# Optimization experiments

Hardware: AMD Instinct MI355X
Metric: run time of the kernel (lower is better)

## Reference

```python
import jax, jax.numpy as jnp
import numpy as np

N_NODES = 100000
N_EDGES = 1600000
IN_DIM, HID_DIM, OUT_DIM = 128, 256, 128


def setup_inputs() -> dict:
    key = jax.random.key(0)
    ks = jax.random.split(key, 5)
    x = jax.random.normal(ks[0], (N_NODES, IN_DIM), dtype=jnp.float32)
    src = jax.random.randint(ks[1], (N_EDGES,), 0, N_NODES, dtype=jnp.int64)
    dst = jax.random.randint(ks[2], (N_EDGES,), 0, N_NODES, dtype=jnp.int64)
    # Glorot-ish init for linear weights (DGL GraphConv default), zero bias
    W1 = jax.random.normal(ks[3], (IN_DIM, HID_DIM), dtype=jnp.float32) * (1.0 / np.sqrt(IN_DIM))
    W2 = jax.random.normal(ks[4], (HID_DIM, OUT_DIM), dtype=jnp.float32) * (1.0 / np.sqrt(HID_DIM))
    b1 = jnp.zeros((HID_DIM,), dtype=jnp.float32)
    b2 = jnp.zeros((OUT_DIM,), dtype=jnp.float32)
    return {"x": x, "src": src, "dst": dst, "W1": W1, "b1": b1, "W2": W2, "b2": b2}


def _degree_norms(src, dst, n_nodes):
    # norm='both': D_out(src)^{-1/2} on messages, D_in(dst)^{-1/2} on aggregate;
    # degrees clamped to min 1 as in DGL.
    ones = jnp.ones(src.shape[0], dtype=jnp.float32)
    deg_out = jax.ops.segment_sum(ones, src, num_segments=n_nodes)
    deg_in = jax.ops.segment_sum(ones, dst, num_segments=n_nodes)
    norm_src = jax.lax.rsqrt(jnp.maximum(deg_out, 1.0))
    norm_dst = jax.lax.rsqrt(jnp.maximum(deg_in, 1.0))
    return norm_src, norm_dst


def _graph_conv(x, src, dst, W, b, norm_src, norm_dst):
    h = x * norm_src[:, None]                                  # [N, d]
    agg = jax.ops.segment_sum(h[src], dst, num_segments=x.shape[0])  # [N, d]
    agg = agg * norm_dst[:, None]
    return agg @ W + b


def reference(x, src, dst, W1, b1, W2, b2):
    norm_src, norm_dst = _degree_norms(src, dst, x.shape[0])
    h = jax.nn.relu(_graph_conv(x, src, dst, W1, b1, norm_src, norm_dst))
    out = _graph_conv(h, src, dst, W2, b2, norm_src, norm_dst)
    return out
```

## Files before the change

kernel.cpp:

```cpp
#include <hip/hip_runtime.h>

constexpr int N_NODES = 100000;
constexpr int N_EDGES = 1600000;
constexpr int DIN = 128, DHID = 256, DOUT = 128;

constexpr int NB = 256;
constexpr int BR = 391;
constexpr int CAP = 8192;
constexpr int NBLK1 = 256;
constexpr int CHUNK = (N_EDGES + NBLK1 - 1) / NBLK1;

typedef __bf16 bf16x8 __attribute__((ext_vector_type(8)));
typedef float f32x4 __attribute__((ext_vector_type(4)));

static __device__ __forceinline__ ushort f2bf(float f) {
    uint u = __float_as_uint(f);
    uint r = (u + 0x7FFFu + ((u >> 16) & 1u)) >> 16;
    return (ushort)r;
}
static __device__ __forceinline__ float bf2f(ushort h) {
    return __uint_as_float(((uint)h) << 16);
}
static __device__ __forceinline__ float bflo(uint w) { return __uint_as_float(w << 16); }
static __device__ __forceinline__ float bfhi(uint w) { return __uint_as_float(w & 0xFFFF0000u); }

__global__ __launch_bounds__(512) void part_kernel(const int* __restrict__ src,
                                                   const int* __restrict__ dst,
                                                   int* __restrict__ curA, int* __restrict__ curB,
                                                   uint* __restrict__ ppair,
                                                   ushort* __restrict__ psv, int e,
                                                   const float* __restrict__ W1,
                                                   ushort* __restrict__ Wf1,
                                                   const float* __restrict__ W2,
                                                   ushort* __restrict__ Wf2) {
    const int t = threadIdx.x;
    if (blockIdx.x >= NBLK1) {
        int i = (blockIdx.x - NBLK1) * 512 + t;
        if (i < DIN * DHID) {
            int frag = i >> 9, r = i & 511;
            int lane = r >> 3, ee = r & 7;
            int kb = frag & 3, ii = (frag >> 2) & 1, w = (frag >> 3) & 3, kh = frag >> 5;
            int c = w * 32 + ii * 16 + (lane & 15);
            int k = kb * 32 + (lane >> 4) * 8 + ee;
            Wf1[i] = f2bf(W1[k * DHID + kh * 128 + c]);
        } else {
            int i2 = i - DIN * DHID;
            int frag = i2 >> 9, r = i2 & 511;
            int lane = r >> 3, ee = r & 7;
            int kb2 = frag & 3, j2 = (frag >> 2) & 1, w = (frag >> 3) & 3, kh = frag >> 5;
            int c2 = w * 32 + j2 * 16 + (lane & 15);
            int k2 = kh * 128 + kb2 * 32 + (lane >> 4) * 8 + ee;
            Wf2[i2] = f2bf(W2[k2 * DOUT + c2]);
        }
        return;
    }
    __shared__ int hA[NB], hB[NB], rA[NB], rB[NB], cA[NB], cB[NB];
    const int b0 = blockIdx.x * CHUNK;
    const int cnt = min(e - b0, CHUNK);
    if (t < NB) { hA[t] = 0; hB[t] = 0; cA[t] = 0; cB[t] = 0; }
    __syncthreads();
    for (int i = t; i < cnt; i += 512) {
        int s = src[b0 + i], d = dst[b0 + i];
        atomicAdd(&hA[d / BR], 1);
        atomicAdd(&hB[s / BR], 1);
    }
    __syncthreads();
    if (t < NB) {
        rA[t] = atomicAdd(&curA[t], hA[t]);
        rB[t] = atomicAdd(&curB[t], hB[t]);
    }
    __syncthreads();
    for (int i = t; i < cnt; i += 512) {
        int s = src[b0 + i], d = dst[b0 + i];
        int bd = d / BR;
        int bs = s / BR;
        int p = rA[bd] + atomicAdd(&cA[bd], 1);
        if (p < CAP) ppair[(size_t)bd * CAP + p] = ((uint)(d - bd * BR) << 17) | (uint)s;
        int q = rB[bs] + atomicAdd(&cB[bs], 1);
        if (q < CAP) psv[(size_t)bs * CAP + q] = (ushort)(s - bs * BR);
    }
}

__global__ __launch_bounds__(512) void csrn_kernel(const int* __restrict__ curA,
                                                   const int* __restrict__ curB,
                                                   const uint* __restrict__ ppair,
                                                   const ushort* __restrict__ psv,
                                                   int* __restrict__ csr,
                                                   int* __restrict__ rowstart,
                                                   float* __restrict__ ndst,
                                                   float* __restrict__ nsrc,
                                                   const float* __restrict__ x,
                                                   ushort* __restrict__ xb, int n, int e) {
    __shared__ uint ploc[CAP];
    __shared__ int hist[512], sc[512], exc[512], cur[512];
    __shared__ int sbst;
    const int t = threadIdx.x;
    const int b = blockIdx.x & 255;
    const int side = blockIdx.x >> 8;
    const int first = b * BR;
    const int nr = min(BR, n - first);
    const size_t base = (size_t)b * CAP;

    if (side == 0) {
        const int cntA = min(curA[b], CAP);
        if (t < 256) sc[t] = curA[t];
        __syncthreads();
        for (int off = 1; off < 256; off <<= 1) {
            int add = 0;
            if (t < 256 && t >= off) add = sc[t - off];
            __syncthreads();
            if (t < 256) sc[t] += add;
            __syncthreads();
        }
        if (t == 0) {
            sbst = (b == 0) ? 0 : sc[b - 1];
            if (b == 0) rowstart[n] = e;
        }
        hist[t] = 0;
        cur[t] = 0;
        __syncthreads();
        const int bst = sbst;

        for (int i = t; i < cntA; i += 512) {
            uint p = ppair[base + i];
            ploc[i] = p;
            atomicAdd(&hist[p >> 17], 1);
        }
        __syncthreads();
        int h = hist[t];
        sc[t] = h;
        __syncthreads();
        for (int off = 1; off < 512; off <<= 1) {
            int add = (t >= off) ? sc[t - off] : 0;
            __syncthreads();
            sc[t] += add;
            __syncthreads();
        }
        exc[t] = sc[t] - h;
        if (t < nr) {
            rowstart[first + t] = bst + exc[t];
            ndst[first + t] = rsqrtf(fmaxf((float)h, 1.0f));
        }
        __syncthreads();
        for (int i = t; i < cntA; i += 512) {
            uint p = ploc[i];
            int dl = p >> 17;
            int pos = exc[dl] + atomicAdd(&cur[dl], 1);
            csr[bst + pos] = (int)(p & 0x1FFFFu);
        }
    } else {
        if (nr <= 0) return;
        hist[t] = 0;
        __syncthreads();
        const int cntB = min(curB[b], CAP);
        for (int i = t; i < cntB; i += 512) atomicAdd(&hist[psv[base + i]], 1);
        __syncthreads();
        float* nsv = (float*)exc;
        if (t < nr) {
            float v = rsqrtf(fmaxf((float)hist[t], 1.0f));
            nsrc[first + t] = v;
            nsv[t] = v;
        }
        __syncthreads();
        const int rl = t >> 5, q = t & 31;
        for (int i = rl; i < nr; i += 16) {
            float s = nsv[i];
            const size_t ro = (size_t)(first + i) * 128;
            float4 v = *(const float4*)&x[ro + q * 4];
            ushort4 o = {f2bf(v.x * s), f2bf(v.y * s), f2bf(v.z * s), f2bf(v.w * s)};
            *(ushort4*)&xb[ro + q * 4] = o;
        }
    }
}

template <bool OUTBF16, bool ADDBIAS>
__global__ __launch_bounds__(256) void aggh_kernel(const ushort* __restrict__ Xb,
                                                   const int* __restrict__ csr,
                                                   const int* __restrict__ rowstart,
                                                   const float* __restrict__ ndst,
                                                   const float* __restrict__ bias,
                                                   float* __restrict__ outf,
                                                   ushort* __restrict__ outb, int n, int half) {
    int g = threadIdx.x >> 3;
    int lane = threadIdx.x & 7;
    int d = blockIdx.x * 32 + g;
    if (d >= n) return;
    int beg = rowstart[d], end = rowstart[d + 1];
    const int fo = half * 64 + lane * 8;
    const ushort* Xp = Xb + fo;
    float acc[8];
#pragma unroll
    for (int j = 0; j < 8; j++) acc[j] = 0.f;

#define ACC8(v)                                   \
    do {                                          \
        acc[0] += bflo(v.x); acc[1] += bfhi(v.x); \
        acc[2] += bflo(v.y); acc[3] += bfhi(v.y); \
        acc[4] += bflo(v.z); acc[5] += bfhi(v.z); \
        acc[6] += bflo(v.w); acc[7] += bfhi(v.w); \
    } while (0)

    int k = beg;
    for (; k + 4 <= end; k += 4) {
        int s0 = csr[k], s1 = csr[k + 1], s2 = csr[k + 2], s3 = csr[k + 3];
        uint4 v0 = *(const uint4*)(Xp + (size_t)s0 * 128);
        uint4 v1 = *(const uint4*)(Xp + (size_t)s1 * 128);
        uint4 v2 = *(const uint4*)(Xp + (size_t)s2 * 128);
        uint4 v3 = *(const uint4*)(Xp + (size_t)s3 * 128);
        ACC8(v0);
        ACC8(v1);
        ACC8(v2);
        ACC8(v3);
    }
    for (; k < end; ++k) {
        uint4 v = *(const uint4*)(Xp + (size_t)csr[k] * 128);
        ACC8(v);
    }
#undef ACC8

    float nd = ndst[d];
#pragma unroll
    for (int j = 0; j < 8; j++) acc[j] *= nd;
    if constexpr (ADDBIAS) {
        float4 b0 = *(const float4*)&bias[fo];
        float4 b1 = *(const float4*)&bias[fo + 4];
        acc[0] += b0.x; acc[1] += b0.y; acc[2] += b0.z; acc[3] += b0.w;
        acc[4] += b1.x; acc[5] += b1.y; acc[6] += b1.z; acc[7] += b1.w;
    }
    if constexpr (OUTBF16) {
        uint4 o;
        o.x = (uint)f2bf(acc[0]) | ((uint)f2bf(acc[1]) << 16);
        o.y = (uint)f2bf(acc[2]) | ((uint)f2bf(acc[3]) << 16);
        o.z = (uint)f2bf(acc[4]) | ((uint)f2bf(acc[5]) << 16);
        o.w = (uint)f2bf(acc[6]) | ((uint)f2bf(acc[7]) << 16);
        *(uint4*)(outb + (size_t)d * 128 + fo) = o;
    } else {
        float4 o0 = {acc[0], acc[1], acc[2], acc[3]};
        float4 o1 = {acc[4], acc[5], acc[6], acc[7]};
        *(float4*)(outf + (size_t)d * 128 + fo) = o0;
        *(float4*)(outf + (size_t)d * 128 + fo + 4) = o1;
    }
}

__global__ __launch_bounds__(256) void fused64_kernel(const ushort* __restrict__ A,
                                                      const ushort* __restrict__ Wf1,
                                                      const float* __restrict__ b1,
                                                      const float* __restrict__ nsrc,
                                                      const ushort* __restrict__ Wf2,
                                                      ushort* __restrict__ T, int M) {
    __shared__ ushort Sa[64][128];
    __shared__ ushort H1[64][128];
    const int row0 = blockIdx.x * 64;
    const int t = threadIdx.x;
    const int w = t >> 6, lane = t & 63;
    const int l16 = lane & 15, lk = lane >> 4;

    float nsv[4];
#pragma unroll
    for (int j = 0; j < 4; j++) {
        int gm = row0 + j * 16 + l16;
        nsv[j] = nsrc[gm < M ? gm : (M - 1)];
    }
    float4 bvv[2][2];
#pragma unroll
    for (int kh = 0; kh < 2; kh++)
#pragma unroll
        for (int i = 0; i < 2; i++)
            bvv[kh][i] = *(const float4*)&b1[kh * 128 + w * 32 + i * 16 + lk * 4];

#pragma unroll
    for (int i = 0; i < 4; i++) {
        int idx = i * 256 + t;
        int r = idx >> 4, oct = idx & 15;
        int gr = row0 + r;
        uint4 v = make_uint4(0u, 0u, 0u, 0u);
        if (gr < M) v = *(const uint4*)&A[(size_t)gr * 128 + oct * 8];
        *(uint4*)((char*)&Sa[0][0] + r * 256 + (oct ^ (r & 15)) * 16) = v;
    }
    __syncthreads();

    f32x4 acc2[4][2];
#pragma unroll
    for (int i = 0; i < 4; i++)
#pragma unroll
        for (int j = 0; j < 2; j++) acc2[i][j] = (f32x4){0.f, 0.f, 0.f, 0.f};

    for (int kh = 0; kh < 2; kh++) {
        const ushort* w1p = Wf1 + ((size_t)(kh * 4 + w) * 8) * 512 + lane * 8;
        const ushort* w2p = Wf2 + ((size_t)(kh * 4 + w) * 8) * 512 + lane * 8;
        bf16x8 af[2][4], wb[2][4];
#pragma unroll
        for (int i = 0; i < 2; i++)
#pragma unroll
            for (int kb = 0; kb < 4; kb++) af[i][kb] = *(const bf16x8*)(w1p + (i * 4 + kb) * 512);
#pragma unroll
        for (int j2 = 0; j2 < 2; j2++)
#pragma unroll
            for (int kb2 = 0; kb2 < 4; kb2++)
                wb[j2][kb2] = *(const bf16x8*)(w2p + (j2 * 4 + kb2) * 512);

        f32x4 acc1[2][4];
#pragma unroll
        for (int i = 0; i < 2; i++)
#pragma unroll
            for (int j = 0; j < 4; j++) acc1[i][j] = (f32x4){0.f, 0.f, 0.f, 0.f};

#pragma unroll
        for (int kb = 0; kb < 4; kb++) {
            bf16x8 bf_[4];
#pragma unroll
            for (int j = 0; j < 4; j++) {
                int m = j * 16 + l16;
                bf_[j] = *(const bf16x8*)((const char*)&Sa[0][0] + m * 256 +
                                          ((kb * 4 + lk) ^ l16) * 16);
            }
#pragma unroll
            for (int i = 0; i < 2; i++)
#pragma unroll
                for (int j = 0; j < 4; j++)
                    acc1[i][j] =
                        __builtin_amdgcn_mfma_f32_16x16x32_bf16(af[i][kb], bf_[j], acc1[i][j], 0, 0, 0);
        }
        __syncthreads();

#pragma unroll
        for (int i = 0; i < 2; i++) {
            int cb = w * 32 + i * 16 + lk * 4;
            float4 bv = bvv[kh][i];
#pragma unroll
            for (int j = 0; j < 4; j++) {
                int m = j * 16 + l16;
                float ns = nsv[j];
                ushort4 pk;
                pk.x = f2bf(fmaxf(acc1[i][j][0] + bv.x, 0.f) * ns);
                pk.y = f2bf(fmaxf(acc1[i][j][1] + bv.y, 0.f) * ns);
                pk.z = f2bf(fmaxf(acc1[i][j][2] + bv.z, 0.f) * ns);
                pk.w = f2bf(fmaxf(acc1[i][j][3] + bv.w, 0.f) * ns);
                int oct = cb >> 3;
                *(ushort4*)((char*)&H1[0][0] + m * 256 + ((oct ^ l16) & 15) * 16 +
                            (cb & 7) * 2) = pk;
            }
        }
        __syncthreads();

#pragma unroll
        for (int kb2 = 0; kb2 < 4; kb2++) {
            bf16x8 ha[4];
#pragma unroll
            for (int i2 = 0; i2 < 4; i2++) {
                int m = i2 * 16 + l16;
                ha[i2] = *(const bf16x8*)((const char*)&H1[0][0] + m * 256 +
                                          ((kb2 * 4 + lk) ^ l16) * 16);
            }
#pragma unroll
            for (int i2 = 0; i2 < 4; i2++)
#pragma unroll
                for (int j2 = 0; j2 < 2; j2++)
                    acc2[i2][j2] = __builtin_amdgcn_mfma_f32_16x16x32_bf16(ha[i2], wb[j2][kb2],
                                                                           acc2[i2][j2], 0, 0, 0);
        }
    }

#pragma unroll
    for (int i2 = 0; i2 < 4; i2++) {
#pragma unroll
        for (int j2 = 0; j2 < 2; j2++) {
#pragma unroll
            for (int q = 0; q < 4; q++) {
                int r = row0 + i2 * 16 + lk * 4 + q;
                int c = w * 32 + j2 * 16 + l16;
                if (r < M) T[(size_t)r * DOUT + c] = f2bf(acc2[i2][j2][q]);
            }
        }
    }
}

extern "C" void kernel_launch(void* const* d_in, const int* in_sizes, int n_in,
                              void* d_out, int out_size, void* d_ws, size_t ws_size,
                              hipStream_t stream) {
    const float* x  = (const float*)d_in[0];
    const int*   src = (const int*)d_in[1];
    const int*   dst = (const int*)d_in[2];
    const float* W1 = (const float*)d_in[3];
    const float* b1 = (const float*)d_in[4];
    const float* W2 = (const float*)d_in[5];
    const float* b2 = (const float*)d_in[6];
    float* out = (float*)d_out;

    const int N = N_NODES, E = N_EDGES;

    size_t off = 0;
    auto carve = [&](size_t bytes) -> void* {
        void* p = (char*)d_ws + off;
        off += (bytes + 255) & ~(size_t)255;
        return p;
    };
    int* curA     = (int*)carve(NB * 4);
    int* curB     = (int*)carve(NB * 4);
    int* rowstart = (int*)carve((size_t)(N + 1) * 4);
    float* ndst   = (float*)carve((size_t)N * 4);
    float* nsrc   = (float*)carve((size_t)N * 4);
    int* csr      = (int*)carve((size_t)E * 4);
    ushort* Wf1   = (ushort*)carve(DIN * DHID * 2);
    ushort* Wf2   = (ushort*)carve(DHID * DOUT * 2);
    ushort* xb    = (ushort*)carve((size_t)N * DIN * 2);
    ushort* agg1b = (ushort*)carve((size_t)N * DIN * 2);
    ushort* tb    = (ushort*)carve((size_t)N * DOUT * 2);
    uint*   ppair = (uint*)carve((size_t)NB * CAP * 4);
    ushort* psv   = (ushort*)carve((size_t)NB * CAP * 2);

    hipMemsetAsync(curA, 0, 2 * NB * 4, stream);

    part_kernel<<<NBLK1 + 128, 512, 0, stream>>>(src, dst, curA, curB, ppair, psv, E,
                                                 W1, Wf1, W2, Wf2);
    csrn_kernel<<<2 * NB, 512, 0, stream>>>(curA, curB, ppair, psv, csr, rowstart, ndst, nsrc,
                                            x, xb, N, E);

    const int gagg = (N + 31) / 32;
    aggh_kernel<true, false><<<gagg, 256, 0, stream>>>(xb, csr, rowstart, ndst, nullptr,
                                                       nullptr, agg1b, N, 0);
    aggh_kernel<true, false><<<gagg, 256, 0, stream>>>(xb, csr, rowstart, ndst, nullptr,
                                                       nullptr, agg1b, N, 1);

    fused64_kernel<<<(N + 63) / 64, 256, 0, stream>>>(agg1b, Wf1, b1, nsrc, Wf2, tb, N);

    aggh_kernel<false, true><<<gagg, 256, 0, stream>>>(tb, csr, rowstart, ndst, b2,
                                                       out, nullptr, N, 0);
    aggh_kernel<false, true><<<gagg, 256, 0, stream>>>(tb, csr, rowstart, ndst, b2,
                                                       out, nullptr, N, 1);
}
```

Before: 207.7 us.

## Merge half-feature aggregation launches, cache edges in registers, unroll gather by eight

Each pair of aggregation launches for the two 64-column halves becomes a single launch with twice the blocks, and each block picks its half from the block index. This removes two kernel launches and the gap between them. The partition kernel keeps the src/dst values it loads in the histogram pass in registers, so the scatter pass does not reload them from global memory. The gather loop also gets an 8-way unrolled stage, which keeps more independent row loads in flight at the cost of extra registers.

```diff
diff --git a/kernel.cpp b/kernel.cpp
--- a/kernel.cpp
+++ b/kernel.cpp
@@ -9,6 +9,7 @@
 constexpr int CAP = 8192;
 constexpr int NBLK1 = 256;
 constexpr int CHUNK = (N_EDGES + NBLK1 - 1) / NBLK1;
+constexpr int NIT = (CHUNK + 511) / 512;
 
 typedef __bf16 bf16x8 __attribute__((ext_vector_type(8)));
 typedef float f32x4 __attribute__((ext_vector_type(4)));
@@ -59,10 +60,17 @@
     const int cnt = min(e - b0, CHUNK);
     if (t < NB) { hA[t] = 0; hB[t] = 0; cA[t] = 0; cB[t] = 0; }
     __syncthreads();
-    for (int i = t; i < cnt; i += 512) {
-        int s = src[b0 + i], d = dst[b0 + i];
-        atomicAdd(&hA[d / BR], 1);
-        atomicAdd(&hB[s / BR], 1);
+
+    int sA[NIT], dA[NIT];
+#pragma unroll
+    for (int i = 0; i < NIT; i++) {
+        int idx = i * 512 + t;
+        if (idx < cnt) {
+            sA[i] = src[b0 + idx];
+            dA[i] = dst[b0 + idx];
+            atomicAdd(&hA[dA[i] / BR], 1);
+            atomicAdd(&hB[sA[i] / BR], 1);
+        }
     }
     __syncthreads();
     if (t < NB) {
@@ -70,14 +78,18 @@
         rB[t] = atomicAdd(&curB[t], hB[t]);
     }
     __syncthreads();
-    for (int i = t; i < cnt; i += 512) {
-        int s = src[b0 + i], d = dst[b0 + i];
-        int bd = d / BR;
-        int bs = s / BR;
-        int p = rA[bd] + atomicAdd(&cA[bd], 1);
-        if (p < CAP) ppair[(size_t)bd * CAP + p] = ((uint)(d - bd * BR) << 17) | (uint)s;
-        int q = rB[bs] + atomicAdd(&cB[bs], 1);
-        if (q < CAP) psv[(size_t)bs * CAP + q] = (ushort)(s - bs * BR);
+#pragma unroll
+    for (int i = 0; i < NIT; i++) {
+        int idx = i * 512 + t;
+        if (idx < cnt) {
+            int s = sA[i], d = dA[i];
+            int bd = d / BR;
+            int bs = s / BR;
+            int p = rA[bd] + atomicAdd(&cA[bd], 1);
+            if (p < CAP) ppair[(size_t)bd * CAP + p] = ((uint)(d - bd * BR) << 17) | (uint)s;
+            int q = rB[bs] + atomicAdd(&cB[bs], 1);
+            if (q < CAP) psv[(size_t)bs * CAP + q] = (ushort)(s - bs * BR);
+        }
     }
 }
 
@@ -180,10 +192,12 @@
                                                    const float* __restrict__ ndst,
                                                    const float* __restrict__ bias,
                                                    float* __restrict__ outf,
-                                                   ushort* __restrict__ outb, int n, int half) {
+                                                   ushort* __restrict__ outb, int n, int G) {
+    const int half = (blockIdx.x >= G) ? 1 : 0;
+    const int bid = blockIdx.x - half * G;
     int g = threadIdx.x >> 3;
     int lane = threadIdx.x & 7;
-    int d = blockIdx.x * 32 + g;
+    int d = bid * 32 + g;
     if (d >= n) return;
     int beg = rowstart[d], end = rowstart[d + 1];
     const int fo = half * 64 + lane * 8;
@@ -201,6 +215,26 @@
     } while (0)
 
     int k = beg;
+    for (; k + 8 <= end; k += 8) {
+        int s0 = csr[k], s1 = csr[k + 1], s2 = csr[k + 2], s3 = csr[k + 3];
+        int s4 = csr[k + 4], s5 = csr[k + 5], s6 = csr[k + 6], s7 = csr[k + 7];
+        uint4 v0 = *(const uint4*)(Xp + (size_t)s0 * 128);
+        uint4 v1 = *(const uint4*)(Xp + (size_t)s1 * 128);
+        uint4 v2 = *(const uint4*)(Xp + (size_t)s2 * 128);
+        uint4 v3 = *(const uint4*)(Xp + (size_t)s3 * 128);
+        uint4 v4 = *(const uint4*)(Xp + (size_t)s4 * 128);
+        uint4 v5 = *(const uint4*)(Xp + (size_t)s5 * 128);
+        uint4 v6 = *(const uint4*)(Xp + (size_t)s6 * 128);
+        uint4 v7 = *(const uint4*)(Xp + (size_t)s7 * 128);
+        ACC8(v0);
+        ACC8(v1);
+        ACC8(v2);
+        ACC8(v3);
+        ACC8(v4);
+        ACC8(v5);
+        ACC8(v6);
+        ACC8(v7);
+    }
     for (; k + 4 <= end; k += 4) {
         int s0 = csr[k], s1 = csr[k + 1], s2 = csr[k + 2], s3 = csr[k + 3];
         uint4 v0 = *(const uint4*)(Xp + (size_t)s0 * 128);
@@ -417,15 +451,11 @@
                                             x, xb, N, E);
 
     const int gagg = (N + 31) / 32;
-    aggh_kernel<true, false><<<gagg, 256, 0, stream>>>(xb, csr, rowstart, ndst, nullptr,
-                                                       nullptr, agg1b, N, 0);
-    aggh_kernel<true, false><<<gagg, 256, 0, stream>>>(xb, csr, rowstart, ndst, nullptr,
-                                                       nullptr, agg1b, N, 1);
+    aggh_kernel<true, false><<<2 * gagg, 256, 0, stream>>>(xb, csr, rowstart, ndst, nullptr,
+                                                           nullptr, agg1b, N, gagg);
 
     fused64_kernel<<<(N + 63) / 64, 256, 0, stream>>>(agg1b, Wf1, b1, nsrc, Wf2, tb, N);
 
-    aggh_kernel<false, true><<<gagg, 256, 0, stream>>>(tb, csr, rowstart, ndst, b2,
-                                                       out, nullptr, N, 0);
-    aggh_kernel<false, true><<<gagg, 256, 0, stream>>>(tb, csr, rowstart, ndst, b2,
-                                                       out, nullptr, N, 1);
-}
+    aggh_kernel<false, true><<<2 * gagg, 256, 0, stream>>>(tb, csr, rowstart, ndst, b2,
+                                                           out, nullptr, N, gagg);
+}
```

New measurement: 197.5 us. -4.9%, faster.
